# Kernel tuning notes

Hardware: AMD Instinct MI355X
Metric: run time of the kernel (lower is better)

The kernel has to match this reference:

```python
import jax, jax.numpy as jnp
import numpy as np

T, N, C, L = 256, 64, 4096, 32
BLANK = 0
NEG = -1e30  # effective log(0)


def setup_inputs() -> dict:
    key = jax.random.key(0)
    k1, k2 = jax.random.split(key)
    preds = jax.random.normal(k1, (T, N, C), dtype=jnp.float32)
    # labels in [1, C): never equal to blank index 0
    targets = jax.random.randint(k2, (N * L,), 1, C, dtype=jnp.int32)
    pred_lengths = jnp.full((N,), T, dtype=jnp.int32)
    target_lengths = jnp.full((N,), L, dtype=jnp.int32)
    return {"preds": preds, "targets": targets,
            "pred_lengths": pred_lengths, "target_lengths": target_lengths}


def _ctc_loss(log_probs, targets2d, pred_lengths, target_lengths):
    # log_probs: (T, N, C); targets2d: (N, L)
    T_, N_, _ = log_probs.shape
    L_ = targets2d.shape[1]
    S = 2 * L_ + 1
    # extended label sequence: blank, l1, blank, l2, ..., blank  -> (N, S)
    ext = jnp.full((N_, S), BLANK, dtype=targets2d.dtype)
    ext = ext.at[:, 1::2].set(targets2d)
    # lp_ext[t, n, s] = log_probs[t, n, ext[n, s]]  -> (T, N, S)
    lp_ext = log_probs[:, jnp.arange(N_)[:, None], ext]
    s_idx = jnp.arange(S)
    # positions beyond this sample's extended length are invalid
    valid_s = s_idx[None, :] < (2 * target_lengths[:, None] + 1)  # (N, S)
    # skip (s-2 -> s) transition allowed only for non-blank labels that differ
    # from the label two positions back
    skip_ok = (s_idx[None, :] >= 2) & (ext != BLANK) & (ext != jnp.roll(ext, 2, axis=1))

    alpha0 = jnp.full((N_, S), NEG, dtype=log_probs.dtype)
    alpha0 = alpha0.at[:, 0].set(lp_ext[0, :, 0])
    alpha0 = alpha0.at[:, 1].set(jnp.where(target_lengths > 0, lp_ext[0, :, 1], NEG))
    alpha0 = jnp.where(valid_s, alpha0, NEG)

    def step(alpha, inp):
        lp_t, t = inp
        a1 = alpha
        a2 = jnp.concatenate([jnp.full((N_, 1), NEG, alpha.dtype), alpha[:, :-1]], axis=1)
        a3 = jnp.concatenate([jnp.full((N_, 2), NEG, alpha.dtype), alpha[:, :-2]], axis=1)
        a3 = jnp.where(skip_ok, a3, NEG)
        comb = jnp.logaddexp(jnp.logaddexp(a1, a2), a3)
        new = jnp.where(valid_s, comb + lp_t, NEG)
        active = (t < pred_lengths)[:, None]  # freeze alpha past sample end
        return jnp.where(active, new, alpha), None

    alphaT, _ = jax.lax.scan(step, alpha0, (lp_ext[1:], jnp.arange(1, T_)))
    end = 2 * target_lengths  # index of final blank in extended sequence
    a_last = jnp.take_along_axis(alphaT, end[:, None], axis=1)[:, 0]
    a_prev = jnp.take_along_axis(alphaT, jnp.maximum(end - 1, 0)[:, None], axis=1)[:, 0]
    a_prev = jnp.where(target_lengths > 0, a_prev, NEG)
    nll = -jnp.logaddexp(a_last, a_prev)
    # zero_infinity=True: zero out infinite / degenerate losses
    nll = jnp.where(jnp.isfinite(nll) & (nll < 1e29), nll, 0.0)
    # reduction='mean': divide each loss by its target length, then batch mean
    return jnp.mean(nll / jnp.maximum(target_lengths, 1).astype(nll.dtype))


def reference(preds, targets, pred_lengths, target_lengths):
    log_probs = jax.nn.log_softmax(preds, axis=2)
    targets2d = targets.reshape(N, L)  # all target_lengths equal L here
    return _ctc_loss(log_probs, targets2d, pred_lengths, target_lengths)
```

## Files before the change

### kernel.cpp

```cpp
#include <hip/hip_runtime.h>
#include <math.h>

#define T_ 256
#define N_ 64
#define C_ 4096
#define L_ 32
#define SL_ 33
#define NEGV (-1e30f)

__device__ __forceinline__ float lae2(float a, float b) {
    float m = fmaxf(a, b);
    return m + __logf(__expf(a - m) + __expf(b - m));
}

__device__ __forceinline__ float dpp_shr1(float x, float fill) {
    int r = __builtin_amdgcn_update_dpp(__float_as_int(fill), __float_as_int(x),
                                        0x138, 0xF, 0xF, false);
    return __int_as_float(r);
}

__device__ __forceinline__ float wred_max(float v) {
    #pragma unroll
    for (int o = 32; o > 0; o >>= 1) v = fmaxf(v, __shfl_xor(v, o));
    return v;
}
__device__ __forceinline__ float wred_sum(float v) {
    #pragma unroll
    for (int o = 32; o > 0; o >>= 1) v += __shfl_xor(v, o);
    return v;
}

__global__ __launch_bounds__(256) void k_row_lse(
        const float* __restrict__ preds, const int* __restrict__ targets,
        float* __restrict__ lp) {
    const int bid = blockIdx.x;
    const int n   = bid & (N_ - 1);
    const int tid = threadIdx.x;
    const float* row = preds + (size_t)bid * C_;

    float gv = 0.f;
    if (tid < SL_) {
        const int cls = (tid == 0) ? 0 : targets[n * L_ + (tid - 1)];
        gv = row[cls];
    }

    float4 v[4];
    #pragma unroll
    for (int k = 0; k < 4; ++k) v[k] = ((const float4*)row)[tid + k * 256];

    float m = v[0].x;
    #pragma unroll
    for (int k = 0; k < 4; ++k)
        m = fmaxf(m, fmaxf(fmaxf(v[k].x, v[k].y), fmaxf(v[k].z, v[k].w)));
    m = wred_max(m);

    __shared__ float red[8];
    const int wave = tid >> 6, lane = tid & 63;
    if (lane == 0) red[wave] = m;
    __syncthreads();
    const float M = fmaxf(fmaxf(red[0], red[1]), fmaxf(red[2], red[3]));

    float s = 0.f;
    #pragma unroll
    for (int k = 0; k < 4; ++k)
        s += __expf(v[k].x - M) + __expf(v[k].y - M)
           + __expf(v[k].z - M) + __expf(v[k].w - M);
    s = wred_sum(s);
    if (lane == 0) red[4 + wave] = s;
    __syncthreads();
    const float lse = M + __logf(red[4] + red[5] + red[6] + red[7]);

    if (tid < SL_) {
        const int t = bid >> 6;
        lp[((size_t)n * T_ + t) * SL_ + tid] = gv - lse;
    }
}

__global__ __launch_bounds__(256) void k_ctc_scan(
        const float* __restrict__ lp, const int* __restrict__ targets,
        const int* __restrict__ plen, const int* __restrict__ tlen,
        float* __restrict__ partial) {
    __shared__ __align__(16) float lds[(T_ + 1) * SL_];
    const int n = blockIdx.x;
    const int tid = threadIdx.x;
    const float4* src = (const float4*)(lp + (size_t)n * T_ * SL_);
    float4* dst = (float4*)lds;
    for (int i = tid; i < (T_ * SL_) / 4; i += 256) dst[i] = src[i];
    __syncthreads();
    if (tid >= 64) return;

    const int lane = tid;
    const int tl = tlen[n];
    const int pl = plen[n];
    const int ends = 2 * tl;
    const bool odd = (lane & 1);
    const int slot   = odd ? 1 + (lane >> 1) : 0;
    const int cls    = odd ? targets[n * L_ + (lane >> 1)] : 0;
    const int clsm2  = (odd && lane >= 2) ? targets[n * L_ + (lane >> 1) - 1] : 0;
    const bool skip  = odd && (lane >= 2) && (cls != 0) && (cls != clsm2);
    const bool valid   = lane < 2 * tl + 1;
    const bool valid64 = (2 * tl + 1) > 64;

    float a = NEGV, b = NEGV;
    if (lane == 0) a = lds[0];
    if (lane == 1 && tl > 0) a = lds[1];

    float lp_s  = lds[SL_ + slot];
    float lp64  = lds[SL_];

    for (int t = 1; t < T_; ++t) {
        const float lp_s_nxt = lds[(t + 1) * SL_ + slot];
        const float lp64_nxt = lds[(t + 1) * SL_];

        const float a2 = dpp_shr1(a, NEGV);
        float a3 = dpp_shr1(a2, NEGV);
        a3 = skip ? a3 : NEGV;
        const float m3 = fmaxf(fmaxf(a, a2), a3);
        const float comb = m3 + __logf(__expf(a - m3) + __expf(a2 - m3)
                                       + __expf(a3 - m3));
        const float nb = valid64 ? (lae2(b, a) + lp64) : NEGV;
        const float na = valid ? (comb + lp_s) : NEGV;
        if (t < pl) { a = na; b = nb; }
        lp_s = lp_s_nxt; lp64 = lp64_nxt;
    }

    const float a_last = (ends >= 64) ? __shfl(b, 63) : __shfl(a, ends);
    float a_prev = __shfl(a, (ends > 0) ? (ends - 1) : 0);
    if (tl <= 0) a_prev = NEGV;
    float nll = -lae2(a_last, a_prev);
    if (!(isfinite(nll) && nll < 1e29f)) nll = 0.f;
    if (lane == 0) partial[n] = nll / (float)((tl > 0) ? tl : 1);
}

__global__ void k_mean(const float* __restrict__ partial, float* __restrict__ out) {
    float v = partial[threadIdx.x];
    v = wred_sum(v);
    if (threadIdx.x == 0) out[0] = v * (1.0f / (float)N_);
}

extern "C" void kernel_launch(void* const* d_in, const int* in_sizes, int n_in,
                              void* d_out, int out_size, void* d_ws, size_t ws_size,
                              hipStream_t stream) {
    const float* preds   = (const float*)d_in[0];
    const int*   targets = (const int*)d_in[1];
    const int*   plen    = (const int*)d_in[2];
    const int*   tlen    = (const int*)d_in[3];

    float* lp      = (float*)d_ws;
    float* partial = lp + (size_t)N_ * T_ * SL_;

    k_row_lse<<<T_ * N_, 256, 0, stream>>>(preds, targets, lp);
    k_ctc_scan<<<N_, 256, 0, stream>>>(lp, targets, plen, tlen, partial);
    k_mean<<<1, 64, 0, stream>>>(partial, (float*)d_out);
}
```

Baseline: 402.2 us.

## Fuse batch mean into scan kernel, prefetch LDS deeper, use nontemporal loads

Result: no change. 396.9 us (-1.3%).

```diff
diff --git a/kernel.cpp b/kernel.cpp
--- a/kernel.cpp
+++ b/kernel.cpp
@@ -7,6 +7,8 @@
 #define L_ 32
 #define SL_ 33
 #define NEGV (-1e30f)
+
+typedef float vf4 __attribute__((ext_vector_type(4)));
 
 __device__ __forceinline__ float lae2(float a, float b) {
     float m = fmaxf(a, b);
@@ -32,10 +34,11 @@
 
 __global__ __launch_bounds__(256) void k_row_lse(
         const float* __restrict__ preds, const int* __restrict__ targets,
-        float* __restrict__ lp) {
+        float* __restrict__ lp, int* __restrict__ counter) {
     const int bid = blockIdx.x;
     const int n   = bid & (N_ - 1);
     const int tid = threadIdx.x;
+    if (bid == 0 && tid == 0) *counter = 0;
     const float* row = preds + (size_t)bid * C_;
 
     float gv = 0.f;
@@ -44,14 +47,16 @@
         gv = row[cls];
     }
 
-    float4 v[4];
-    #pragma unroll
-    for (int k = 0; k < 4; ++k) v[k] = ((const float4*)row)[tid + k * 256];
-
-    float m = v[0].x;
+    const vf4* row4 = (const vf4*)row;
+    vf4 v[4];
     #pragma unroll
     for (int k = 0; k < 4; ++k)
-        m = fmaxf(m, fmaxf(fmaxf(v[k].x, v[k].y), fmaxf(v[k].z, v[k].w)));
+        v[k] = __builtin_nontemporal_load(&row4[tid + k * 256]);
+
+    float m = v[0][0];
+    #pragma unroll
+    for (int k = 0; k < 4; ++k)
+        m = fmaxf(m, fmaxf(fmaxf(v[k][0], v[k][1]), fmaxf(v[k][2], v[k][3])));
     m = wred_max(m);
 
     __shared__ float red[8];
@@ -63,8 +68,8 @@
     float s = 0.f;
     #pragma unroll
     for (int k = 0; k < 4; ++k)
-        s += __expf(v[k].x - M) + __expf(v[k].y - M)
-           + __expf(v[k].z - M) + __expf(v[k].w - M);
+        s += __expf(v[k][0] - M) + __expf(v[k][1] - M)
+           + __expf(v[k][2] - M) + __expf(v[k][3] - M);
     s = wred_sum(s);
     if (lane == 0) red[4 + wave] = s;
     __syncthreads();
@@ -79,12 +84,13 @@
 __global__ __launch_bounds__(256) void k_ctc_scan(
         const float* __restrict__ lp, const int* __restrict__ targets,
         const int* __restrict__ plen, const int* __restrict__ tlen,
-        float* __restrict__ partial) {
-    __shared__ __align__(16) float lds[(T_ + 1) * SL_];
+        float* __restrict__ partial, int* __restrict__ counter,
+        float* __restrict__ out) {
+    __shared__ __align__(16) float lds[(T_ + 16) * SL_];
     const int n = blockIdx.x;
     const int tid = threadIdx.x;
-    const float4* src = (const float4*)(lp + (size_t)n * T_ * SL_);
-    float4* dst = (float4*)lds;
+    const vf4* src = (const vf4*)(lp + (size_t)n * T_ * SL_);
+    vf4* dst = (vf4*)lds;
     for (int i = tid; i < (T_ * SL_) / 4; i += 256) dst[i] = src[i];
     __syncthreads();
     if (tid >= 64) return;
@@ -105,23 +111,31 @@
     if (lane == 0) a = lds[0];
     if (lane == 1 && tl > 0) a = lds[1];
 
-    float lp_s  = lds[SL_ + slot];
-    float lp64  = lds[SL_];
+    float pf_s[4], pf_b[4];
+    #pragma unroll
+    for (int j = 0; j < 4; ++j) {
+        pf_s[j] = lds[(1 + j) * SL_ + slot];
+        pf_b[j] = lds[(1 + j) * SL_];
+    }
+    for (int t = 1; t <= T_; t += 4) {
+        #pragma unroll
+        for (int j = 0; j < 4; ++j) {
+            const float lp_s = pf_s[j];
+            const float lp64 = pf_b[j];
+            pf_s[j] = lds[(t + 4 + j) * SL_ + slot];
+            pf_b[j] = lds[(t + 4 + j) * SL_];
 
-    for (int t = 1; t < T_; ++t) {
-        const float lp_s_nxt = lds[(t + 1) * SL_ + slot];
-        const float lp64_nxt = lds[(t + 1) * SL_];
-
-        const float a2 = dpp_shr1(a, NEGV);
-        float a3 = dpp_shr1(a2, NEGV);
-        a3 = skip ? a3 : NEGV;
-        const float m3 = fmaxf(fmaxf(a, a2), a3);
-        const float comb = m3 + __logf(__expf(a - m3) + __expf(a2 - m3)
-                                       + __expf(a3 - m3));
-        const float nb = valid64 ? (lae2(b, a) + lp64) : NEGV;
-        const float na = valid ? (comb + lp_s) : NEGV;
-        if (t < pl) { a = na; b = nb; }
-        lp_s = lp_s_nxt; lp64 = lp64_nxt;
+            const float a2 = dpp_shr1(a, NEGV);
+            float a3 = dpp_shr1(a2, NEGV);
+            a3 = skip ? a3 : NEGV;
+            const float m3 = fmaxf(fmaxf(a, a2), a3);
+            const float comb = m3 + __logf(__expf(a - m3) + __expf(a2 - m3)
+                                           + __expf(a3 - m3));
+            const float nb = valid64 ? (lae2(b, a) + lp64) : NEGV;
+            const float na = valid ? (comb + lp_s) : NEGV;
+            const int tt = t + j;
+            if (tt < pl) { a = na; b = nb; }
+        }
     }
 
     const float a_last = (ends >= 64) ? __shfl(b, 63) : __shfl(a, ends);
@@ -130,12 +144,17 @@
     float nll = -lae2(a_last, a_prev);
     if (!(isfinite(nll) && nll < 1e29f)) nll = 0.f;
     if (lane == 0) partial[n] = nll / (float)((tl > 0) ? tl : 1);
-}
 
-__global__ void k_mean(const float* __restrict__ partial, float* __restrict__ out) {
-    float v = partial[threadIdx.x];
-    v = wred_sum(v);
-    if (threadIdx.x == 0) out[0] = v * (1.0f / (float)N_);
+    __threadfence();
+    int done = 0;
+    if (lane == 0) done = atomicAdd(counter, 1);
+    done = __shfl(done, 0);
+    if (done == N_ - 1) {
+        __threadfence();
+        float v = partial[lane];
+        v = wred_sum(v);
+        if (lane == 0) out[0] = v * (1.0f / (float)N_);
+    }
 }
 
 extern "C" void kernel_launch(void* const* d_in, const int* in_sizes, int n_in,
@@ -148,8 +167,9 @@
 
     float* lp      = (float*)d_ws;
     float* partial = lp + (size_t)N_ * T_ * SL_;
+    int*   counter = (int*)(partial + N_);
 
-    k_row_lse<<<T_ * N_, 256, 0, stream>>>(preds, targets, lp);
-    k_ctc_scan<<<N_, 256, 0, stream>>>(lp, targets, plen, tlen, partial);
-    k_mean<<<1, 64, 0, stream>>>(partial, (float*)d_out);
+    k_row_lse<<<T_ * N_, 256, 0, stream>>>(preds, targets, lp, counter);
+    k_ctc_scan<<<N_, 256, 0, stream>>>(lp, targets, plen, tlen, partial,
+                                       counter, (float*)d_out);
 }
```
